# Kernel tuning notes

Measured on AMD Instinct MI355X. Metric: run time of the kernel, lower is better.

## Reference

```python
import jax, jax.numpy as jnp
import numpy as np

DIM = 1024
NUM_HEADS = 16
HEAD_DIM = DIM // NUM_HEADS
SCALE = HEAD_DIM ** -0.5


def setup_inputs() -> dict:
    key = jax.random.key(0)
    k_x, k_qkv, k_pw, k_pb = jax.random.split(key, 4)
    B, S = 2, 2048
    x = jax.random.normal(k_x, (B, S, DIM), dtype=jnp.float32)
    # nn.Linear(dim, 3*dim, bias=False): weight [3*dim, dim]
    w_qkv = jax.random.normal(k_qkv, (3 * DIM, DIM), dtype=jnp.float32) * (DIM ** -0.5)
    # nn.Linear(dim, dim): weight [dim, dim], bias [dim]
    w_proj = jax.random.normal(k_pw, (DIM, DIM), dtype=jnp.float32) * (DIM ** -0.5)
    b_proj = jax.random.normal(k_pb, (DIM,), dtype=jnp.float32) * 0.01
    return {"x": x, "w_qkv": w_qkv, "w_proj": w_proj, "b_proj": b_proj}


def reference(x, w_qkv, w_proj, b_proj):
    B, S, D = x.shape
    qkv = jnp.einsum("bsd,ed->bse", x, w_qkv)  # [B,S,3D]
    q, k, v = jnp.split(qkv, 3, axis=-1)
    def heads(t):  # [B,S,D] -> [B,H,S,hd]
        return t.reshape(B, S, NUM_HEADS, HEAD_DIM).transpose(0, 2, 1, 3)
    q, k, v = heads(q), heads(k), heads(v)
    attn = jnp.einsum("bhqd,bhkd->bhqk", q, k) * SCALE  # [B,H,S,S]
    attn = jax.nn.softmax(attn, axis=-1)
    out = jnp.einsum("bhqk,bhkd->bhqd", attn, v)  # [B,H,S,hd]
    out = out.transpose(0, 2, 1, 3).reshape(B, S, D)
    return jnp.einsum("bsd,ed->bse", out, w_proj) + b_proj
```

## Files before the change

### kernel.cpp

```cpp
#include <hip/hip_runtime.h>
#include <stdint.h>

typedef __bf16 bf16;
typedef __bf16 bf16x8 __attribute__((ext_vector_type(8)));
typedef float f32x4 __attribute__((ext_vector_type(4)));
typedef float f32x16 __attribute__((ext_vector_type(16)));

typedef __attribute__((address_space(1))) void gvoid_t;
typedef __attribute__((address_space(3))) void lvoid_t;

__device__ __forceinline__ void gload16(const void* src, void* lds) {
    __builtin_amdgcn_global_load_lds((gvoid_t*)src, (lvoid_t*)lds, 16, 0, 0);
}

__device__ __forceinline__ float fexp2(float x) {
    float r;
    asm("v_exp_f32 %0, %1" : "=v"(r) : "v"(x));
    return r;
}

__global__ __launch_bounds__(256) void cvt3_kernel(const float* __restrict__ x,
                                                   const float* __restrict__ wqkv,
                                                   const float* __restrict__ wproj,
                                                   bf16* __restrict__ xb,
                                                   bf16* __restrict__ wqkvb,
                                                   bf16* __restrict__ wprojb) {
    int idx = blockIdx.x * 256 + threadIdx.x;
    int stride = gridDim.x * 256;
    for (int i = idx; i < 1048576; i += stride) {
        const float* in;
        bf16* out;
        int j;
        if (i < 524288) { in = x; out = xb; j = i; }
        else if (i < 917504) { in = wqkv; out = wqkvb; j = i - 524288; }
        else { in = wproj; out = wprojb; j = i - 917504; }
        const float4* p = (const float4*)in;
        float4 a = p[(long)j * 2], b = p[(long)j * 2 + 1];
        bf16x8 o;
        o[0] = (bf16)a.x; o[1] = (bf16)a.y; o[2] = (bf16)a.z; o[3] = (bf16)a.w;
        o[4] = (bf16)b.x; o[5] = (bf16)b.y; o[6] = (bf16)b.z; o[7] = (bf16)b.w;
        ((bf16x8*)out)[j] = o;
    }
}

template <bool F32OUT, int BN>
__global__ __launch_bounds__(256) void gemm_bt(const bf16* __restrict__ A,
                                               const bf16* __restrict__ W,
                                               const float* __restrict__ bias,
                                               void* __restrict__ Cout,
                                               const int M, const int N, const int K) {
    constexpr int NT = BN / 32;
    __shared__ __align__(16) bf16 Alds[4096];
    __shared__ __align__(16) bf16 Blds[4096];
    const int t = threadIdx.x;
    const int wid = t >> 6, lane = t & 63;
    const int g = lane >> 4, c = lane & 15;
    const int wm = wid >> 1, wn = wid & 1;
    const long bm = (long)blockIdx.y * 128, bn = (long)blockIdx.x * BN;

    f32x4 acc[4][NT] = {};

    const int arow = t >> 2;
    const int acol = (t & 3) * 8;
    const bf16* Asrc = A + (bm + arow) * (long)K + acol;
    const bf16* Bsrc = W + (bn + arow) * (long)K + acol;
    bf16* adst = Alds + wid * 512;
    bf16* bdst = Blds + wid * 512;

    for (int k0 = 0; k0 < K; k0 += 32) {
        gload16(Asrc + k0, adst);
        gload16(Asrc + k0 + (long)64 * K, adst + 2048);
        gload16(Bsrc + k0, bdst);
        if constexpr (BN == 128)
            gload16(Bsrc + k0 + (long)64 * K, bdst + 2048);
        __syncthreads();
        bf16x8 af[4], bfr[NT];
#pragma unroll
        for (int mt = 0; mt < 4; ++mt)
            af[mt] = *(const bf16x8*)(Alds + (wm * 64 + mt * 16 + c) * 32 + g * 8);
#pragma unroll
        for (int nt = 0; nt < NT; ++nt)
            bfr[nt] = *(const bf16x8*)(Blds + (wn * (BN / 2) + nt * 16 + c) * 32 + g * 8);
#pragma unroll
        for (int mt = 0; mt < 4; ++mt)
#pragma unroll
            for (int nt = 0; nt < NT; ++nt)
                acc[mt][nt] = __builtin_amdgcn_mfma_f32_16x16x32_bf16(af[mt], bfr[nt],
                                                                      acc[mt][nt], 0, 0, 0);
        __syncthreads();
    }
#pragma unroll
    for (int mt = 0; mt < 4; ++mt) {
#pragma unroll
        for (int nt = 0; nt < NT; ++nt) {
#pragma unroll
            for (int i = 0; i < 4; ++i) {
                const long row = bm + wm * 64 + mt * 16 + g * 4 + i;
                const long col = bn + wn * (BN / 2) + nt * 16 + c;
                if constexpr (F32OUT) {
                    ((float*)Cout)[row * N + col] = acc[mt][nt][i] + bias[col];
                } else {
                    ((bf16*)Cout)[row * N + col] = (bf16)acc[mt][nt][i];
                }
            }
        }
    }
}

__global__ __launch_bounds__(256) void vtrans_kernel(const bf16* __restrict__ qkv,
                                                     bf16* __restrict__ Vt) {
    __shared__ float Lf[64 * 65];
    const int t = threadIdx.x;
    const int bid = blockIdx.x;
    const int b = bid >> 9, r = bid & 511;
    const int s0 = (r & 31) * 64, hd0 = (r >> 5) * 64;

    const int sr = t >> 3, scol = (t & 7) * 8;
    const bf16* src = qkv + (long)(b * 2048 + s0 + sr) * 3072 + 2048 + hd0 + scol;
    bf16x8 v0 = *(const bf16x8*)src;
    bf16x8 v1 = *(const bf16x8*)(src + (long)32 * 3072);
#pragma unroll
    for (int e = 0; e < 8; ++e) {
        Lf[(scol + e) * 65 + sr] = (float)v0[e];
        Lf[(scol + e) * 65 + sr + 32] = (float)v1[e];
    }
    __syncthreads();
    const int hr = t >> 2, ss = (t & 3) * 16;
    bf16 outv[16];
#pragma unroll
    for (int j = 0; j < 16; ++j) outv[j] = (bf16)Lf[hr * 65 + ss + j];
    bf16* dst = Vt + ((long)b * 1024 + hd0 + hr) * 2048 + s0 + ss;
    *(bf16x8*)dst = *(bf16x8*)outv;
    *(bf16x8*)(dst + 8) = *(bf16x8*)(outv + 8);
}

__global__ __launch_bounds__(256) void flash_kernel(const bf16* __restrict__ qkv,
                                                    const bf16* __restrict__ Vt,
                                                    bf16* __restrict__ attno) {
    __shared__ __align__(16) bf16 KV[24576];
    __shared__ float LP[128];

    const int t = threadIdx.x;
    const int wid = t >> 6, lane = t & 63;
    const int l31 = lane & 31, hl = lane >> 5;

    const int i0 = blockIdx.x;
    const int xcd = i0 & 7, slot = i0 >> 3;
    const int bh = xcd * 4 + (slot >> 4);
    const int qb = slot & 15;
    const int b = bh >> 4, h = bh & 15;
    const int rowbase = b * 2048;
    const int q0w = qb * 128 + wid * 32;

    bf16x8 qf[4];
    {
        const bf16* qrow = qkv + (long)(rowbase + q0w + l31) * 3072 + h * 64 + hl * 8;
        const float qs = 0.18033688f;
#pragma unroll
        for (int ks = 0; ks < 4; ++ks) {
            bf16x8 a = *(const bf16x8*)(qrow + ks * 16);
#pragma unroll
            for (int e = 0; e < 8; ++e) qf[ks][e] = (bf16)((float)a[e] * qs);
        }
    }

    const bf16* ksn = qkv + (long)(rowbase + (wid >> 1) * 32 + l31) * 3072 + 1024 + h * 64 +
                      (wid & 1) * 32 + hl * 8;
    const bf16* vsn = Vt + ((long)b * 1024 + h * 64 + (wid >> 1) * 32 + l31) * 2048 +
                      (wid & 1) * 32 + hl * 8;
    const int kchunk = wid * 1024;

    float lpA = 0.f, lpB = 0.f, lpC = 0.f, lpD = 0.f;
    f32x16 oacc0 = {}, oacc1 = {};

#define STAGE(BI)                                                        \
    {                                                                    \
        bf16* kd = KV + (BI) * 4096 + kchunk;                            \
        bf16* vd = KV + 12288 + (BI) * 4096 + kchunk;                    \
        gload16(ksn, kd);                                                \
        gload16(ksn + 16, kd + 512);                                     \
        gload16(vsn, vd);                                                \
        gload16(vsn + 16, vd + 512);                                     \
        ksn += 196608;                                                   \
        vsn += 64;                                                       \
    }

    const bf16* kl;
    const bf16* vl;

    auto compute = [&](int bi) __attribute__((always_inline)) {
        kl = KV + bi * 4096 + lane * 8;
        vl = KV + 12288 + bi * 4096 + lane * 8;
        f32x16 s0 = {}, s1 = {};
        __builtin_amdgcn_s_setprio(1);
#pragma unroll
        for (int ks = 0; ks < 4; ++ks) {
            bf16x8 kf0 = *(const bf16x8*)(kl + ks * 512);
            bf16x8 kf1 = *(const bf16x8*)(kl + 2048 + ks * 512);
            s0 = __builtin_amdgcn_mfma_f32_32x32x16_bf16(kf0, qf[ks], s0, 0, 0, 0);
            s1 = __builtin_amdgcn_mfma_f32_32x32x16_bf16(kf1, qf[ks], s1, 0, 0, 0);
        }
        __builtin_amdgcn_s_setprio(0);
        float p0[16], p1[16];
#pragma unroll
        for (int r = 0; r < 16; ++r) p0[r] = fexp2(s0[r]);
#pragma unroll
        for (int r = 0; r < 16; ++r) p1[r] = fexp2(s1[r]);
#pragma unroll
        for (int r = 0; r < 4; ++r) {
            lpA += p0[r * 4 + 0] + p1[r * 4 + 0];
            lpB += p0[r * 4 + 1] + p1[r * 4 + 1];
            lpC += p0[r * 4 + 2] + p1[r * 4 + 2];
            lpD += p0[r * 4 + 3] + p1[r * 4 + 3];
        }
        __builtin_amdgcn_s_setprio(1);
#pragma unroll
        for (int ks = 0; ks < 4; ++ks) {
            const float* pp = (ks < 2) ? p0 : p1;
            const int s = (ks & 1) * 8;
            unsigned wA, wB, wC, wD;
            asm("v_cvt_pk_bf16_f32 %0, %1, %2" : "=v"(wA) : "v"(pp[s + 0]), "v"(pp[s + 1]));
            asm("v_cvt_pk_bf16_f32 %0, %1, %2" : "=v"(wB) : "v"(pp[s + 4]), "v"(pp[s + 5]));
            asm("v_cvt_pk_bf16_f32 %0, %1, %2" : "=v"(wC) : "v"(pp[s + 2]), "v"(pp[s + 3]));
            asm("v_cvt_pk_bf16_f32 %0, %1, %2" : "=v"(wD) : "v"(pp[s + 6]), "v"(pp[s + 7]));
            asm("v_permlane32_swap_b32 %0, %1" : "+v"(wA), "+v"(wB));
            asm("v_permlane32_swap_b32 %0, %1" : "+v"(wC), "+v"(wD));
            union { unsigned w[4]; bf16x8 v; } pu;
            pu.w[0] = wA; pu.w[1] = wC; pu.w[2] = wB; pu.w[3] = wD;
            bf16x8 vf0 = *(const bf16x8*)(vl + ks * 512);
            bf16x8 vf1 = *(const bf16x8*)(vl + 2048 + ks * 512);
            oacc0 = __builtin_amdgcn_mfma_f32_32x32x16_bf16(pu.v, vf0, oacc0, 0, 0, 0);
            oacc1 = __builtin_amdgcn_mfma_f32_32x32x16_bf16(pu.v, vf1, oacc1, 0, 0, 0);
        }
        __builtin_amdgcn_s_setprio(0);
    };

    STAGE(0);
    STAGE(1);

#define FSTEP(CUR, NXT)                                    \
    asm volatile("s_waitcnt vmcnt(4)" ::: "memory");       \
    __builtin_amdgcn_s_barrier();                          \
    STAGE(NXT);                                            \
    compute(CUR);

    for (int t3 = 0; t3 < 10; ++t3) {
        FSTEP(0, 2)
        FSTEP(1, 0)
        FSTEP(2, 1)
    }
    asm volatile("s_waitcnt vmcnt(4)" ::: "memory");
    __builtin_amdgcn_s_barrier();
    compute(0);
    asm volatile("s_waitcnt vmcnt(0)" ::: "memory");
    __builtin_amdgcn_s_barrier();
    compute(1);
#undef FSTEP
#undef STAGE

    float lpart = (lpA + lpB) + (lpC + lpD);
    lpart += __shfl_xor(lpart, 32);
    if (lane < 32) LP[wid * 32 + l31] = lpart;
    float inv[16];
#pragma unroll
    for (int r = 0; r < 16; ++r) {
        const int qrow = (r & 3) + 8 * (r >> 2) + 4 * hl;
        inv[r] = 1.0f / LP[wid * 32 + qrow];
    }

#pragma unroll
    for (int r = 0; r < 16; ++r) {
        const int qrow = (r & 3) + 8 * (r >> 2) + 4 * hl;
        const long rbase = (long)(rowbase + q0w + qrow) * 1024 + h * 64 + l31;
        attno[rbase] = (bf16)(oacc0[r] * inv[r]);
        attno[rbase + 32] = (bf16)(oacc1[r] * inv[r]);
    }
}

extern "C" void kernel_launch(void* const* d_in, const int* in_sizes, int n_in,
                              void* d_out, int out_size, void* d_ws, size_t ws_size,
                              hipStream_t stream) {
    const float* x = (const float*)d_in[0];
    const float* wqkv = (const float*)d_in[1];
    const float* wproj = (const float*)d_in[2];
    const float* bproj = (const float*)d_in[3];

    char* ws = (char*)d_ws;
    bf16* xb     = (bf16*)(ws);
    bf16* Vt     = (bf16*)(ws);
    bf16* wqkvb  = (bf16*)(ws + 8388608);
    bf16* wprojb = (bf16*)(ws + 14680064);
    bf16* qkv    = (bf16*)(ws + 16777216);
    bf16* attno  = (bf16*)(ws + 41943040);
    if (ws_size < 50331648) return;

    cvt3_kernel<<<2048, 256, 0, stream>>>(x, wqkv, wproj, xb, wqkvb, wprojb);

    gemm_bt<false, 128><<<dim3(24, 32), 256, 0, stream>>>(xb, wqkvb, nullptr, qkv,
                                                          4096, 3072, 1024);

    vtrans_kernel<<<1024, 256, 0, stream>>>(qkv, Vt);

    flash_kernel<<<512, 256, 0, stream>>>(qkv, Vt, attno);

    gemm_bt<true, 64><<<dim3(16, 32), 256, 0, stream>>>(attno, wprojb, bproj, d_out,
                                                        4096, 1024, 1024);
}
```

Before: 128.2 us.

## Triple-buffer GEMM loads and compute V transposed directly via swapped GEMM

The GEMM main loop now uses three LDS buffers with async global-to-LDS loads and vmcnt waits, so the next tiles load while the current one computes, replacing the two syncthreads per k-step. The separate V transpose kernel is gone: the QK projection is computed as a 2048-wide GEMM, and V^T is produced directly by a second GEMM with the operands swapped (Wv x X^T). Flash attention is adjusted for the new qk stride and Vt layout, and the s_setprio hints are removed. The cost is three times the GEMM LDS footprint, which may lower occupancy, plus an extra GEMM launch.

```diff
diff --git a/kernel.cpp b/kernel.cpp
--- a/kernel.cpp
+++ b/kernel.cpp
@@ -50,8 +50,9 @@
                                                void* __restrict__ Cout,
                                                const int M, const int N, const int K) {
     constexpr int NT = BN / 32;
-    __shared__ __align__(16) bf16 Alds[4096];
-    __shared__ __align__(16) bf16 Blds[4096];
+    constexpr int BELEMS = BN * 32;
+    __shared__ __align__(16) bf16 Alds[3 * 4096];
+    __shared__ __align__(16) bf16 Blds[3 * BELEMS];
     const int t = threadIdx.x;
     const int wid = t >> 6, lane = t & 63;
     const int g = lane >> 4, c = lane & 15;
@@ -64,31 +65,65 @@
     const int acol = (t & 3) * 8;
     const bf16* Asrc = A + (bm + arow) * (long)K + acol;
     const bf16* Bsrc = W + (bn + arow) * (long)K + acol;
-    bf16* adst = Alds + wid * 512;
-    bf16* bdst = Blds + wid * 512;
-
-    for (int k0 = 0; k0 < K; k0 += 32) {
-        gload16(Asrc + k0, adst);
-        gload16(Asrc + k0 + (long)64 * K, adst + 2048);
-        gload16(Bsrc + k0, bdst);
-        if constexpr (BN == 128)
-            gload16(Bsrc + k0 + (long)64 * K, bdst + 2048);
-        __syncthreads();
+    const int dstb = wid * 512;
+
+#define GSTAGE(BI)                                                       \
+    {                                                                    \
+        bf16* ad = Alds + (BI) * 4096 + dstb;                            \
+        bf16* bd = Blds + (BI) * BELEMS + dstb;                          \
+        gload16(Asrc, ad);                                               \
+        gload16(Asrc + (long)64 * K, ad + 2048);                         \
+        gload16(Bsrc, bd);                                               \
+        if constexpr (BN == 128) gload16(Bsrc + (long)64 * K, bd + 2048);\
+        Asrc += 32;                                                      \
+        Bsrc += 32;                                                      \
+    }
+
+    auto computeg = [&](int bi) __attribute__((always_inline)) {
+        const bf16* Ab = Alds + bi * 4096;
+        const bf16* Bb = Blds + bi * BELEMS;
         bf16x8 af[4], bfr[NT];
 #pragma unroll
         for (int mt = 0; mt < 4; ++mt)
-            af[mt] = *(const bf16x8*)(Alds + (wm * 64 + mt * 16 + c) * 32 + g * 8);
+            af[mt] = *(const bf16x8*)(Ab + (wm * 64 + mt * 16 + c) * 32 + g * 8);
 #pragma unroll
         for (int nt = 0; nt < NT; ++nt)
-            bfr[nt] = *(const bf16x8*)(Blds + (wn * (BN / 2) + nt * 16 + c) * 32 + g * 8);
+            bfr[nt] = *(const bf16x8*)(Bb + (wn * (BN / 2) + nt * 16 + c) * 32 + g * 8);
 #pragma unroll
         for (int mt = 0; mt < 4; ++mt)
 #pragma unroll
             for (int nt = 0; nt < NT; ++nt)
                 acc[mt][nt] = __builtin_amdgcn_mfma_f32_16x16x32_bf16(af[mt], bfr[nt],
                                                                       acc[mt][nt], 0, 0, 0);
-        __syncthreads();
-    }
+    };
+
+#define GWAITN                                                              \
+    if constexpr (BN == 128) { asm volatile("s_waitcnt vmcnt(4)" ::: "memory"); } \
+    else { asm volatile("s_waitcnt vmcnt(3)" ::: "memory"); }
+
+#define GSTEP(CUR, NXT)            \
+    GWAITN;                        \
+    __builtin_amdgcn_s_barrier();  \
+    GSTAGE(NXT);                   \
+    computeg(CUR);
+
+    GSTAGE(0);
+    GSTAGE(1);
+    for (int t3 = 0; t3 < 10; ++t3) {
+        GSTEP(0, 2)
+        GSTEP(1, 0)
+        GSTEP(2, 1)
+    }
+    GWAITN;
+    __builtin_amdgcn_s_barrier();
+    computeg(0);
+    asm volatile("s_waitcnt vmcnt(0)" ::: "memory");
+    __builtin_amdgcn_s_barrier();
+    computeg(1);
+#undef GSTEP
+#undef GWAITN
+#undef GSTAGE
+
 #pragma unroll
     for (int mt = 0; mt < 4; ++mt) {
 #pragma unroll
@@ -107,34 +142,7 @@
     }
 }
 
-__global__ __launch_bounds__(256) void vtrans_kernel(const bf16* __restrict__ qkv,
-                                                     bf16* __restrict__ Vt) {
-    __shared__ float Lf[64 * 65];
-    const int t = threadIdx.x;
-    const int bid = blockIdx.x;
-    const int b = bid >> 9, r = bid & 511;
-    const int s0 = (r & 31) * 64, hd0 = (r >> 5) * 64;
-
-    const int sr = t >> 3, scol = (t & 7) * 8;
-    const bf16* src = qkv + (long)(b * 2048 + s0 + sr) * 3072 + 2048 + hd0 + scol;
-    bf16x8 v0 = *(const bf16x8*)src;
-    bf16x8 v1 = *(const bf16x8*)(src + (long)32 * 3072);
-#pragma unroll
-    for (int e = 0; e < 8; ++e) {
-        Lf[(scol + e) * 65 + sr] = (float)v0[e];
-        Lf[(scol + e) * 65 + sr + 32] = (float)v1[e];
-    }
-    __syncthreads();
-    const int hr = t >> 2, ss = (t & 3) * 16;
-    bf16 outv[16];
-#pragma unroll
-    for (int j = 0; j < 16; ++j) outv[j] = (bf16)Lf[hr * 65 + ss + j];
-    bf16* dst = Vt + ((long)b * 1024 + hd0 + hr) * 2048 + s0 + ss;
-    *(bf16x8*)dst = *(bf16x8*)outv;
-    *(bf16x8*)(dst + 8) = *(bf16x8*)(outv + 8);
-}
-
-__global__ __launch_bounds__(256) void flash_kernel(const bf16* __restrict__ qkv,
+__global__ __launch_bounds__(256) void flash_kernel(const bf16* __restrict__ qk,
                                                     const bf16* __restrict__ Vt,
                                                     bf16* __restrict__ attno) {
     __shared__ __align__(16) bf16 KV[24576];
@@ -154,7 +162,7 @@
 
     bf16x8 qf[4];
     {
-        const bf16* qrow = qkv + (long)(rowbase + q0w + l31) * 3072 + h * 64 + hl * 8;
+        const bf16* qrow = qk + (long)(rowbase + q0w + l31) * 2048 + h * 64 + hl * 8;
         const float qs = 0.18033688f;
 #pragma unroll
         for (int ks = 0; ks < 4; ++ks) {
@@ -164,9 +172,9 @@
         }
     }
 
-    const bf16* ksn = qkv + (long)(rowbase + (wid >> 1) * 32 + l31) * 3072 + 1024 + h * 64 +
+    const bf16* ksn = qk + (long)(rowbase + (wid >> 1) * 32 + l31) * 2048 + 1024 + h * 64 +
                       (wid & 1) * 32 + hl * 8;
-    const bf16* vsn = Vt + ((long)b * 1024 + h * 64 + (wid >> 1) * 32 + l31) * 2048 +
+    const bf16* vsn = Vt + (long)(h * 64 + (wid >> 1) * 32 + l31) * 4096 + b * 2048 +
                       (wid & 1) * 32 + hl * 8;
     const int kchunk = wid * 1024;
 
@@ -181,18 +189,14 @@
         gload16(ksn + 16, kd + 512);                                     \
         gload16(vsn, vd);                                                \
         gload16(vsn + 16, vd + 512);                                     \
-        ksn += 196608;                                                   \
+        ksn += 131072;                                                   \
         vsn += 64;                                                       \
     }
 
-    const bf16* kl;
-    const bf16* vl;
-
     auto compute = [&](int bi) __attribute__((always_inline)) {
-        kl = KV + bi * 4096 + lane * 8;
-        vl = KV + 12288 + bi * 4096 + lane * 8;
+        const bf16* kl = KV + bi * 4096 + lane * 8;
+        const bf16* vl = KV + 12288 + bi * 4096 + lane * 8;
         f32x16 s0 = {}, s1 = {};
-        __builtin_amdgcn_s_setprio(1);
 #pragma unroll
         for (int ks = 0; ks < 4; ++ks) {
             bf16x8 kf0 = *(const bf16x8*)(kl + ks * 512);
@@ -200,7 +204,6 @@
             s0 = __builtin_amdgcn_mfma_f32_32x32x16_bf16(kf0, qf[ks], s0, 0, 0, 0);
             s1 = __builtin_amdgcn_mfma_f32_32x32x16_bf16(kf1, qf[ks], s1, 0, 0, 0);
         }
-        __builtin_amdgcn_s_setprio(0);
         float p0[16], p1[16];
 #pragma unroll
         for (int r = 0; r < 16; ++r) p0[r] = fexp2(s0[r]);
@@ -213,7 +216,6 @@
             lpC += p0[r * 4 + 2] + p1[r * 4 + 2];
             lpD += p0[r * 4 + 3] + p1[r * 4 + 3];
         }
-        __builtin_amdgcn_s_setprio(1);
 #pragma unroll
         for (int ks = 0; ks < 4; ++ks) {
             const float* pp = (ks < 2) ? p0 : p1;
@@ -232,7 +234,6 @@
             oacc0 = __builtin_amdgcn_mfma_f32_32x32x16_bf16(pu.v, vf0, oacc0, 0, 0, 0);
             oacc1 = __builtin_amdgcn_mfma_f32_32x32x16_bf16(pu.v, vf1, oacc1, 0, 0, 0);
         }
-        __builtin_amdgcn_s_setprio(0);
     };
 
     STAGE(0);
@@ -287,21 +288,22 @@
 
     char* ws = (char*)d_ws;
     bf16* xb     = (bf16*)(ws);
-    bf16* Vt     = (bf16*)(ws);
     bf16* wqkvb  = (bf16*)(ws + 8388608);
     bf16* wprojb = (bf16*)(ws + 14680064);
-    bf16* qkv    = (bf16*)(ws + 16777216);
+    bf16* qk     = (bf16*)(ws + 16777216);
+    bf16* Vt     = (bf16*)(ws + 33554432);
     bf16* attno  = (bf16*)(ws + 41943040);
     if (ws_size < 50331648) return;
 
     cvt3_kernel<<<2048, 256, 0, stream>>>(x, wqkv, wproj, xb, wqkvb, wprojb);
 
-    gemm_bt<false, 128><<<dim3(24, 32), 256, 0, stream>>>(xb, wqkvb, nullptr, qkv,
-                                                          4096, 3072, 1024);
-
-    vtrans_kernel<<<1024, 256, 0, stream>>>(qkv, Vt);
-
-    flash_kernel<<<512, 256, 0, stream>>>(qkv, Vt, attno);
+    gemm_bt<false, 128><<<dim3(16, 32), 256, 0, stream>>>(xb, wqkvb, nullptr, qk,
+                                                          4096, 2048, 1024);
+
+    gemm_bt<false, 64><<<dim3(64, 8), 256, 0, stream>>>(wqkvb + 2048 * 1024, xb, nullptr, Vt,
+                                                        1024, 4096, 1024);
+
+    flash_kernel<<<512, 256, 0, stream>>>(qk, Vt, attno);
 
     gemm_bt<true, 64><<<dim3(16, 32), 256, 0, stream>>>(attno, wprojb, bproj, d_out,
                                                         4096, 1024, 1024);
```

After: 130.3 us. About the same (+1.7%).
